# Performance work log

Hardware: AMD Instinct MI355X
Metric: run time of the kernel (lower is better)

The kernel has to match this reference:

```python
import jax, jax.numpy as jnp
import numpy as np

V, D, DFF, E, K, L = 32000, 1024, 4096, 8, 2, 2
B, S = 2, 1024


def _layer_norm(x, scale, bias, eps=1e-5):
    mu = jnp.mean(x, axis=-1, keepdims=True)
    var = jnp.var(x, axis=-1, keepdims=True)
    return (x - mu) * jax.lax.rsqrt(var + eps) * scale + bias


def setup_inputs() -> dict:
    key = jax.random.key(0)
    ks = jax.random.split(key, 16)
    s = 0.02
    return {
        "input_ids": jax.random.randint(ks[0], (B, S), 0, V, dtype=jnp.int32),
        "emb": jax.random.normal(ks[1], (V, D), jnp.float32) * s,
        "t_ln_scale": jnp.ones((L, D), jnp.float32),
        "t_ln_bias": jnp.zeros((L, D), jnp.float32),
        "t_w1": jax.random.normal(ks[2], (L, D, DFF), jnp.float32) * s,
        "t_b1": jnp.zeros((L, DFF), jnp.float32),
        "t_w2": jax.random.normal(ks[3], (L, DFF, D), jnp.float32) * s,
        "t_b2": jnp.zeros((L, D), jnp.float32),
        "Wr": jax.random.normal(ks[4], (D, E), jnp.float32) * s,
        "br": jnp.zeros((E,), jnp.float32),
        "e_w1": jax.random.normal(ks[5], (E, D, DFF), jnp.float32) * s,
        "e_b1": jnp.zeros((E, DFF), jnp.float32),
        "e_w2": jax.random.normal(ks[6], (E, DFF, D), jnp.float32) * s,
        "e_b2": jnp.zeros((E, D), jnp.float32),
        "Wl": jax.random.normal(ks[7], (D, V), jnp.float32) * s,
        "bl": jnp.zeros((V,), jnp.float32),
    }


def reference(input_ids, emb, t_ln_scale, t_ln_bias, t_w1, t_b1, t_w2, t_b2,
              Wr, br, e_w1, e_b1, e_w2, e_b2, Wl, bl):
    # token embeddings: [B,S,D]
    x = emb[input_ids]

    # temporal abstraction: L pre-LN residual MLP blocks
    for l in range(L):
        h = _layer_norm(x, t_ln_scale[l], t_ln_bias[l])
        h = jax.nn.gelu(jnp.einsum('bsd,df->bsf', h, t_w1[l]) + t_b1[l])
        x = x + jnp.einsum('bsf,fd->bsd', h, t_w2[l]) + t_b2[l]

    # router: top-k renormalized softmax over experts, scattered to [B,S,E]
    r_logits = jnp.einsum('bsd,de->bse', x, Wr) + br
    top_vals, top_idx = jax.lax.top_k(r_logits, K)
    top_w = jax.nn.softmax(top_vals, axis=-1)
    routing_weights = jnp.put_along_axis(
        jnp.zeros_like(r_logits), top_idx, top_w, axis=-1, inplace=False)

    # dense all-experts stack: [B,S,E,D]
    h = jax.nn.gelu(jnp.einsum('bsd,edf->bsef', x, e_w1) + e_b1)
    expert_out = jnp.einsum('bsef,efd->bsed', h, e_w2) + e_b2

    # sparse-weighted combine
    y = jnp.einsum('bse,bsed->bsd', routing_weights, expert_out)

    logits = jnp.einsum('bsd,dv->bsv', y, Wl) + bl
    return logits, routing_weights
```

## Files before the change

kernel.cpp:

```cpp
#include <hip/hip_runtime.h>
#include <stdint.h>

typedef __bf16 bf16;
typedef __bf16 bf16x8 __attribute__((ext_vector_type(8)));
typedef float f32x4 __attribute__((ext_vector_type(4)));

#define DEV __device__ __forceinline__

static constexpr int Dm   = 1024;
static constexpr int DFFm = 4096;
static constexpr int Tm   = 2048;
static constexpr int Vm   = 32000;

#define GLOAD_LDS16(g, l)                                                      \
  __builtin_amdgcn_global_load_lds(                                            \
      (const __attribute__((address_space(1))) unsigned int*)(g),              \
      (__attribute__((address_space(3))) unsigned int*)(l), 16, 0, 0)

DEV float gelu_tanh(float v) {
  float u = 0.7978845608028654f * (v + 0.044715f * v * v * v);
  float e = __expf(2.0f * u);
  float t = 1.0f - 2.0f / (e + 1.0f);
  return 0.5f * v * (1.0f + t);
}

enum { EPI_GELU_SPLIT = 0, EPI_RESID = 1, EPI_GELU_BF16 = 2, EPI_MOE = 3, EPI_BIAS = 4 };

struct GemmP {
  const bf16* Ah;
  const bf16* Bh;
  const float* bias;
  const float* rwp;
  const int* cnt;
  const int* idx;
  float* outF;
  bf16* outH;
  int K; int N;
  int lda; int ldb; int ldo;
  long aBS, bBS, outBS;
  int biasBS;
  int ebase;
  int kcShift; int kcK;
};

template <int EPI, bool GATHER, bool SWZ>
__launch_bounds__(256, 2)
__global__ void gemm_bt(GemmP p) {
  __shared__ bf16 lds[16384];
  bf16* ldsA = lds;
  bf16* ldsB = lds + 8192;

  const int tid  = threadIdx.x;
  const int lane = tid & 63;
  const int wid  = tid >> 6;
  const int wr   = wid >> 1;
  const int wc   = wid & 1;
  const int z    = blockIdx.z;
  const int kc   = z & ((1 << p.kcShift) - 1);
  const int ze   = z >> p.kcShift;

  int bx = blockIdx.x, by = blockIdx.y;
  if constexpr (SWZ) {
    const int gx = gridDim.x, gy = gridDim.y;
    const int nwg = gx * gy;
    const int lin = by * gx + bx;
    const int q = nwg >> 3, r = nwg & 7;
    const int xcd = lin & 7, loc = lin >> 3;
    const int nid = (xcd < r ? xcd * (q + 1) : r * (q + 1) + (xcd - r) * q) + loc;
    bx = nid / gy; by = nid % gy;
  }

  const long am0 = (long)by * 128;
  const long bn0 = (long)bx * 128;

  int cntE = 0;
  const int* il = nullptr;
  if constexpr (GATHER || EPI == EPI_MOE) {
    cntE = p.cnt[p.ebase + ze];
    if (am0 >= cntE) return;
    il = p.idx + (long)(p.ebase + ze) * 2048;
  }

  const long lda = p.lda, ldb = p.ldb;
  const long K = p.K;
  const long kco = (long)kc * p.kcK;

  const int sub = (lane & 7) ^ (lane >> 3);
  const int rIn = wid * 8 + (lane >> 3);

  const bf16 *aS[4], *bS[4];
  {
    const bf16* Bb = p.Bh + (long)ze * p.bBS + kco + bn0 * ldb;
    const bf16* Ab = p.Ah + (long)ze * p.aBS + kco + am0 * lda;
#pragma unroll
    for (int j = 0; j < 4; ++j) {
      const int row = j * 32 + rIn;
      bS[j] = Bb + (long)row * ldb + sub * 8;
      if constexpr (GATHER) {
        const int rt = (int)am0 + row;
        const long grow = il[rt < cntE ? rt : 0];
        aS[j] = p.Ah + grow * lda + kco + sub * 8;
      } else {
        aS[j] = Ab + (long)row * lda + sub * 8;
      }
    }
  }
  char* dstA[4];
#pragma unroll
  for (int j = 0; j < 4; ++j)
    dstA[j] = (char*)(void*)lds + (j * 256 + wid * 64) * 16;

  f32x4 acc[4][4] = {};

  const int r15 = lane & 15;
  const int kcs = lane >> 4;
  const int xk  = lane & 7;

  for (long k0 = 0; k0 < K; k0 += 64) {
    __syncthreads();
#pragma unroll
    for (int j = 0; j < 4; ++j) {
      GLOAD_LDS16(aS[j] + k0, dstA[j]);
      GLOAD_LDS16(bS[j] + k0, dstA[j] + 16384);
    }
    __syncthreads();
#pragma unroll
    for (int h = 0; h < 2; ++h) {
      const int q8 = ((kcs + 4 * h) ^ xk) << 3;
      bf16x8 a[4], b[4];
#pragma unroll
      for (int m = 0; m < 4; ++m)
        a[m] = *(const bf16x8*)(ldsA + (wr * 64 + m * 16 + r15) * 64 + q8);
#pragma unroll
      for (int n = 0; n < 4; ++n)
        b[n] = *(const bf16x8*)(ldsB + (wc * 64 + n * 16 + r15) * 64 + q8);
#pragma unroll
      for (int m = 0; m < 4; ++m)
#pragma unroll
        for (int n = 0; n < 4; ++n)
          acc[m][n] = __builtin_amdgcn_mfma_f32_16x16x32_bf16(a[m], b[n], acc[m][n], 0, 0, 0);
    }
  }

  const long N = p.N;

#pragma unroll
  for (int m = 0; m < 4; ++m) {
#pragma unroll
    for (int n = 0; n < 4; ++n) {
      const long col = bn0 + wc * 64 + n * 16 + (lane & 15);
      const float bv = (kc == 0) ? p.bias[(long)ze * p.biasBS + col] : 0.0f;
#pragma unroll
      for (int r = 0; r < 4; ++r) {
        const long row = am0 + wr * 64 + m * 16 + (lane >> 4) * 4 + r;
        float v = acc[m][n][r] + bv;
        if constexpr (EPI == EPI_GELU_SPLIT) {
          float g = gelu_tanh(v);
          bf16 hh = (bf16)g;
          long o = row * (long)p.ldo + col;
          p.outH[o] = hh;
          p.outH[o + N] = (bf16)(g - (float)hh);
          p.outH[o + 2 * N] = hh;
        } else if constexpr (EPI == EPI_RESID) {
          atomicAdd(p.outF + row * N + col, v);
        } else if constexpr (EPI == EPI_GELU_BF16) {
          long o = (long)ze * p.outBS + row * N + col;
          p.outH[o] = (bf16)gelu_tanh(v);
        } else if constexpr (EPI == EPI_MOE) {
          if (row < cntE) {
            const int tok = il[row];
            const float wgt = p.rwp[(long)tok * 8 + p.ebase + ze];
            atomicAdd(p.outF + (long)tok * N + col, wgt * v);
          }
        } else {
          p.outF[row * N + col] = v;
        }
      }
    }
  }
}

template <bool SWZ>
__launch_bounds__(512, 2)
__global__ void gemm256_bias(const bf16* __restrict__ A, const bf16* __restrict__ B,
                             const float* __restrict__ bias, float* __restrict__ out,
                             int Kc, int Nc) {
  __shared__ bf16 lds[65536];

  const int tid  = threadIdx.x;
  const int lane = tid & 63;
  const int wid  = tid >> 6;
  const int wr   = wid >> 2;
  const int wc   = wid & 3;

  int bx = blockIdx.x, by = blockIdx.y;
  if constexpr (SWZ) {
    const int gx = gridDim.x, gy = gridDim.y;
    const int nwg = gx * gy;
    const int lin = by * gx + bx;
    const int q = nwg >> 3, r = nwg & 7;
    const int xcd = lin & 7, loc = lin >> 3;
    const int nid = (xcd < r ? xcd * (q + 1) : r * (q + 1) + (xcd - r) * q) + loc;
    bx = nid / gy; by = nid % gy;
  }
  const long am0 = (long)by * 256;
  const long bn0 = (long)bx * 256;
  const long K = Kc;
  const int NT = Kc >> 6;

  const int sub = (lane & 7) ^ (lane >> 3);
  const int rw  = wid * 8 + (lane >> 3);
  const bf16 *aS[4], *bS[4];
#pragma unroll
  for (int j = 0; j < 4; ++j) {
    const int row = j * 64 + rw;
    aS[j] = A + (am0 + row) * K + sub * 8;
    bS[j] = B + (bn0 + row) * K + sub * 8;
  }

  f32x4 acc[8][4] = {};
  const int r15 = lane & 15;
  const int kcs = lane >> 4;
  const int xk  = lane & 7;

  auto stage = [&](int kt, int buf) {
    const long ko = (long)kt * 64;
    char* base = (char*)(void*)lds + buf * 65536;
#pragma unroll
    for (int j = 0; j < 4; ++j) {
      char* d = base + (j * 64 + wid * 8) * 128;
      GLOAD_LDS16(aS[j] + ko, d);
      GLOAD_LDS16(bS[j] + ko, d + 32768);
    }
  };

  stage(0, 0);
  stage(1, 1);

  for (int kt = 0; kt < NT; ++kt) {
    const int cur = kt & 1;
    if (kt < NT - 1) asm volatile("s_waitcnt vmcnt(8)" ::: "memory");
    else             asm volatile("s_waitcnt vmcnt(0)" ::: "memory");
    __builtin_amdgcn_s_barrier();

    const bf16* LA = lds + cur * 32768;
    const bf16* LB = LA + 16384;

    bf16x8 a0[8], b0[4];
    {
      const int q8 = (kcs ^ xk) << 3;
#pragma unroll
      for (int m = 0; m < 8; ++m)
        a0[m] = *(const bf16x8*)(LA + (wr * 128 + m * 16 + r15) * 64 + q8);
#pragma unroll
      for (int n = 0; n < 4; ++n)
        b0[n] = *(const bf16x8*)(LB + (wc * 64 + n * 16 + r15) * 64 + q8);
    }
    __builtin_amdgcn_s_setprio(1);
#pragma unroll
    for (int m = 0; m < 8; ++m)
#pragma unroll
      for (int n = 0; n < 4; ++n)
        acc[m][n] = __builtin_amdgcn_mfma_f32_16x16x32_bf16(a0[m], b0[n], acc[m][n], 0, 0, 0);
    __builtin_amdgcn_s_setprio(0);

    bf16x8 a1[8], b1[4];
    {
      const int q8 = ((kcs + 4) ^ xk) << 3;
#pragma unroll
      for (int m = 0; m < 8; ++m)
        a1[m] = *(const bf16x8*)(LA + (wr * 128 + m * 16 + r15) * 64 + q8);
#pragma unroll
      for (int n = 0; n < 4; ++n)
        b1[n] = *(const bf16x8*)(LB + (wc * 64 + n * 16 + r15) * 64 + q8);
    }
    asm volatile("s_waitcnt lgkmcnt(0)" ::: "memory");
    __builtin_amdgcn_s_barrier();
    if (kt + 2 < NT) stage(kt + 2, cur);

    __builtin_amdgcn_s_setprio(1);
#pragma unroll
    for (int m = 0; m < 8; ++m)
#pragma unroll
      for (int n = 0; n < 4; ++n)
        acc[m][n] = __builtin_amdgcn_mfma_f32_16x16x32_bf16(a1[m], b1[n], acc[m][n], 0, 0, 0);
    __builtin_amdgcn_s_setprio(0);
  }

  const long N = Nc;
#pragma unroll
  for (int m = 0; m < 8; ++m) {
#pragma unroll
    for (int n = 0; n < 4; ++n) {
      const long col = bn0 + wc * 64 + n * 16 + r15;
      const float bv = bias[col];
#pragma unroll
      for (int r = 0; r < 4; ++r) {
        const long row = am0 + wr * 128 + m * 16 + (lane >> 4) * 4 + r;
        out[row * N + col] = acc[m][n][r] + bv;
      }
    }
  }
}

template <bool AUG>
__global__ void transpose_cvt(const float* __restrict__ in, bf16* __restrict__ out,
                              int R, int C, long inBS, long outBS) {
  __shared__ float tile[32][33];
  const float* inp = in + (long)blockIdx.z * inBS;
  const long c0 = (long)blockIdx.x * 32;
  const long r0 = (long)blockIdx.y * 32;
  const int tx = threadIdx.x;
  const int ty = threadIdx.y;
#pragma unroll
  for (int i = 0; i < 4; ++i) {
    int r = ty + i * 8;
    tile[r][tx] = inp[(r0 + r) * (long)C + c0 + tx];
  }
  __syncthreads();
  const long ob = (long)blockIdx.z * outBS;
  const long stride = AUG ? 3L * R : (long)R;
#pragma unroll
  for (int i = 0; i < 4; ++i) {
    int c = ty + i * 8;
    float v = tile[tx][c];
    bf16 h = (bf16)v;
    long o = ob + (c0 + c) * stride + r0 + tx;
    out[o] = h;
    if constexpr (AUG) {
      out[o + R] = h;
      out[o + 2 * R] = (bf16)(v - (float)h);
    }
  }
}

__global__ void embed_kernel(const int* __restrict__ ids, const float* __restrict__ emb,
                             float* __restrict__ x) {
  const long t = blockIdx.x;
  const int id = ids[t];
  ((float4*)(x + t * 1024))[threadIdx.x] = ((const float4*)(emb + (long)id * 1024))[threadIdx.x];
}

__global__ void ln_aug_kernel(const float* __restrict__ x, const float* __restrict__ sc,
                              const float* __restrict__ bi, bf16* __restrict__ oa) {
  const long t = blockIdx.x;
  const int tid = threadIdx.x;
  const int lane = tid & 63, wid = tid >> 6;
  float4 a = ((const float4*)(x + t * 1024))[tid];
  float s = a.x + a.y + a.z + a.w;
  float q = a.x * a.x + a.y * a.y + a.z * a.z + a.w * a.w;
#pragma unroll
  for (int off = 32; off; off >>= 1) {
    s += __shfl_down(s, off);
    q += __shfl_down(q, off);
  }
  __shared__ float sr[4], qr[4];
  if (lane == 0) { sr[wid] = s; qr[wid] = q; }
  __syncthreads();
  s = sr[0] + sr[1] + sr[2] + sr[3];
  q = qr[0] + qr[1] + qr[2] + qr[3];
  const float mu = s * (1.0f / 1024.0f);
  const float var = q * (1.0f / 1024.0f) - mu * mu;
  const float rs = rsqrtf(var + 1e-5f);
#pragma unroll
  for (int j = 0; j < 4; ++j) {
    const int d = tid * 4 + j;
    const float g = (((const float*)&a)[j] - mu) * rs * sc[d] + bi[d];
    const bf16 h = (bf16)g;
    oa[t * 3072 + d] = h;
    oa[t * 3072 + 1024 + d] = (bf16)(g - (float)h);
    oa[t * 3072 + 2048 + d] = h;
  }
}

__global__ void router_kernel(const float* __restrict__ x, const float* __restrict__ Wr,
                              const float* __restrict__ br, float* __restrict__ rwo,
                              int* __restrict__ top2) {
  const long t = blockIdx.x;
  const int lane = threadIdx.x;
  float acc[8];
#pragma unroll
  for (int e = 0; e < 8; ++e) acc[e] = 0.0f;
  const float4* xr = (const float4*)(x + t * 1024);
#pragma unroll
  for (int j = 0; j < 4; ++j) {
    const int d4 = j * 64 + lane;
    float4 xv = xr[d4];
#pragma unroll
    for (int u = 0; u < 4; ++u) {
      const float xs = ((const float*)&xv)[u];
      const float4* wp = (const float4*)(Wr + (long)(d4 * 4 + u) * 8);
      float4 w0 = wp[0], w1 = wp[1];
      acc[0] += xs * w0.x; acc[1] += xs * w0.y; acc[2] += xs * w0.z; acc[3] += xs * w0.w;
      acc[4] += xs * w1.x; acc[5] += xs * w1.y; acc[6] += xs * w1.z; acc[7] += xs * w1.w;
    }
  }
#pragma unroll
  for (int off = 32; off; off >>= 1)
#pragma unroll
    for (int e = 0; e < 8; ++e) acc[e] += __shfl_down(acc[e], off);
  if (lane == 0) {
    float v[8];
#pragma unroll
    for (int e = 0; e < 8; ++e) v[e] = acc[e] + br[e];
    int i0 = 0; float v0 = v[0];
    for (int e = 1; e < 8; ++e) if (v[e] > v0) { v0 = v[e]; i0 = e; }
    int i1 = -1; float v1 = -3.4e38f;
    for (int e = 0; e < 8; ++e) if (e != i0 && v[e] > v1) { v1 = v[e]; i1 = e; }
    float e1 = expf(v1 - v0);
    float den = 1.0f + e1;
    float w0 = 1.0f / den, w1 = e1 / den;
    float* o = rwo + t * 8;
#pragma unroll
    for (int e = 0; e < 8; ++e) o[e] = (e == i0) ? w0 : (e == i1 ? w1 : 0.0f);
    top2[t] = i0 | (i1 << 8);
  }
}

__global__ void build_lists(const int* __restrict__ top2, int* __restrict__ cnt,
                            int* __restrict__ idx) {
  const int t = blockIdx.x * 256 + threadIdx.x;
  const int rec = top2[t];
  const int e0 = rec & 255, e1 = (rec >> 8) & 255;
  int p0 = atomicAdd(&cnt[e0], 1);
  idx[e0 * 2048 + p0] = t;
  int p1 = atomicAdd(&cnt[e1], 1);
  idx[e1 * 2048 + p1] = t;
}

__global__ void cvt_bf16_kernel(const float* __restrict__ in, bf16* __restrict__ out, long n) {
  long i = ((long)blockIdx.x * blockDim.x + threadIdx.x) * 8;
  if (i >= n) return;
  float4 a = *(const float4*)(in + i);
  float4 b = *(const float4*)(in + i + 4);
  bf16x8 o;
  o[0] = (bf16)a.x; o[1] = (bf16)a.y; o[2] = (bf16)a.z; o[3] = (bf16)a.w;
  o[4] = (bf16)b.x; o[5] = (bf16)b.y; o[6] = (bf16)b.z; o[7] = (bf16)b.w;
  *(bf16x8*)(out + i) = o;
}

extern "C" void kernel_launch(void* const* d_in, const int* in_sizes, int n_in,
                              void* d_out, int out_size, void* d_ws, size_t ws_size,
                              hipStream_t stream) {
  (void)in_sizes; (void)n_in; (void)out_size; (void)ws_size;
  const int*   ids  = (const int*)d_in[0];
  const float* emb  = (const float*)d_in[1];
  const float* tlns = (const float*)d_in[2];
  const float* tlnb = (const float*)d_in[3];
  const float* tw1  = (const float*)d_in[4];
  const float* tb1  = (const float*)d_in[5];
  const float* tw2  = (const float*)d_in[6];
  const float* tb2  = (const float*)d_in[7];
  const float* Wr   = (const float*)d_in[8];
  const float* br   = (const float*)d_in[9];
  const float* ew1  = (const float*)d_in[10];
  const float* eb1  = (const float*)d_in[11];
  const float* ew2  = (const float*)d_in[12];
  const float* eb2  = (const float*)d_in[13];
  const float* Wl   = (const float*)d_in[14];
  const float* bl   = (const float*)d_in[15];

  float* logits = (float*)d_out;
  float* rwout  = (float*)d_out + (long)Tm * Vm;

  size_t off = 0;
  auto take = [&](size_t bytes) {
    void* pp = (char*)d_ws + off;
    off += (bytes + 255) & ~(size_t)255;
    return pp;
  };
  float* X    = (float*)take((size_t)Tm * Dm * 4);
  bf16*  XB   = (bf16*) take((size_t)Tm * Dm * 2);
  float* Y    = (float*)take((size_t)Tm * Dm * 4);
  bf16*  YB   = (bf16*) take((size_t)Tm * Dm * 2);
  int*   top2 = (int*)  take((size_t)Tm * 4);
  int*   cnt  = (int*)  take(8 * 4);
  int*   idxl = (int*)  take((size_t)8 * Tm * 4);
  char*  S    = (char*) take(134217728);

  bf16* A1  = (bf16*)S;
  bf16* W1A = (bf16*)(S + 12582912);
  bf16* W2A = (bf16*)(S + 12582912 + 25165824);
  bf16* HTA = (bf16*)(S + 12582912 + 2 * 25165824);
  bf16* EW1T = (bf16*)S;
  bf16* HE   = (bf16*)(S + 33554432);
  bf16* EW2T = (bf16*)(S + 100663296);
  bf16* WLT  = (bf16*)S;

  embed_kernel<<<dim3(Tm), dim3(256), 0, stream>>>(ids, emb, X);

  for (int l = 0; l < 2; ++l) {
    transpose_cvt<true><<<dim3(DFFm / 32, Dm / 32, 1), dim3(32, 8), 0, stream>>>(
        tw1 + (long)l * Dm * DFFm, W1A, Dm, DFFm, 0, 0);
    transpose_cvt<true><<<dim3(Dm / 32, DFFm / 32, 1), dim3(32, 8), 0, stream>>>(
        tw2 + (long)l * DFFm * Dm, W2A, DFFm, Dm, 0, 0);
    ln_aug_kernel<<<dim3(Tm), dim3(256), 0, stream>>>(X, tlns + l * Dm, tlnb + l * Dm, A1);

    GemmP p1{};
    p1.Ah = A1; p1.Bh = W1A;
    p1.bias = tb1 + (long)l * DFFm;
    p1.outH = HTA;
    p1.K = 3072; p1.N = DFFm; p1.lda = 3072; p1.ldb = 3072; p1.ldo = 3 * DFFm;
    gemm_bt<EPI_GELU_SPLIT, false, true>
        <<<dim3(DFFm / 128, Tm / 128, 1), dim3(256), 0, stream>>>(p1);

    GemmP p2{};
    p2.Ah = HTA; p2.Bh = W2A;
    p2.bias = tb2 + (long)l * Dm;
    p2.outF = X;
    p2.K = 1536; p2.N = Dm; p2.lda = 12288; p2.ldb = 12288;
    p2.kcShift = 3; p2.kcK = 1536;
    gemm_bt<EPI_RESID, false, true>
        <<<dim3(Dm / 128, Tm / 128, 8), dim3(256), 0, stream>>>(p2);
  }

  router_kernel<<<dim3(Tm), dim3(64), 0, stream>>>(X, Wr, br, rwout, top2);
  hipMemsetAsync(cnt, 0, 8 * 4, stream);
  build_lists<<<dim3(Tm / 256), dim3(256), 0, stream>>>(top2, cnt, idxl);
  cvt_bf16_kernel<<<dim3(Tm * Dm / (256 * 8)), dim3(256), 0, stream>>>(X, XB, (long)Tm * Dm);
  hipMemsetAsync(Y, 0, (size_t)Tm * Dm * 4, stream);

  for (int q = 0; q < 2; ++q) {
    transpose_cvt<false><<<dim3(DFFm / 32, Dm / 32, 4), dim3(32, 8), 0, stream>>>(
        ew1 + (long)q * 4 * Dm * DFFm, EW1T, Dm, DFFm, (long)Dm * DFFm, (long)DFFm * Dm);
    transpose_cvt<false><<<dim3(Dm / 32, DFFm / 32, 4), dim3(32, 8), 0, stream>>>(
        ew2 + (long)q * 4 * DFFm * Dm, EW2T, DFFm, Dm, (long)DFFm * Dm, (long)Dm * DFFm);

    GemmP pe1{};
    pe1.Ah = XB; pe1.Bh = EW1T;
    pe1.bias = eb1 + (long)q * 4 * DFFm; pe1.biasBS = DFFm;
    pe1.outH = HE; pe1.outBS = (long)Tm * DFFm;
    pe1.aBS = 0; pe1.bBS = (long)DFFm * Dm;
    pe1.cnt = cnt; pe1.idx = idxl; pe1.ebase = q * 4;
    pe1.K = Dm; pe1.N = DFFm; pe1.lda = Dm; pe1.ldb = Dm;
    gemm_bt<EPI_GELU_BF16, true, true>
        <<<dim3(DFFm / 128, Tm / 128, 4), dim3(256), 0, stream>>>(pe1);

    GemmP pe2{};
    pe2.Ah = HE; pe2.aBS = (long)Tm * DFFm;
    pe2.Bh = EW2T; pe2.bBS = (long)Dm * DFFm;
    pe2.bias = eb2 + (long)q * 4 * Dm; pe2.biasBS = Dm;
    pe2.rwp = rwout; pe2.cnt = cnt; pe2.idx = idxl; pe2.ebase = q * 4;
    pe2.outF = Y;
    pe2.K = 1024; pe2.N = Dm; pe2.lda = DFFm; pe2.ldb = DFFm;
    pe2.kcShift = 2; pe2.kcK = 1024;
    gemm_bt<EPI_MOE, false, true>
        <<<dim3(Dm / 128, Tm / 128, 16), dim3(256), 0, stream>>>(pe2);
  }

  cvt_bf16_kernel<<<dim3(Tm * Dm / (256 * 8)), dim3(256), 0, stream>>>(Y, YB, (long)Tm * Dm);
  transpose_cvt<false><<<dim3(Vm / 32, Dm / 32, 1), dim3(32, 8), 0, stream>>>(
      Wl, WLT, Dm, Vm, 0, 0);
  gemm256_bias<true><<<dim3(Vm / 256, Tm / 256, 1), dim3(512), 0, stream>>>(
      YB, WLT, bl, logits, Dm, Vm);
}
```

Measured before the change: 980.5 us.

## Move temporal MLP GEMMs to 256-tile kernel with two-term split-bf16 operands

Replaces the 3-way augmented split-bf16 scheme (hi, lo, hi) with a 2-way layout (hi, lo). Virtual K-index remapping lets the GEMM pair A-hi/lo against B-hi twice, which cuts the stored operand width. The temporal MLP GEMMs move to a generalized 256x256-tile kernel with split-K atomics. The first GEMM now writes fp32 to a zeroed scratch buffer, followed by a separate GELU+split pass. This adds a memset and an extra round trip through memory for the activation, and the staging loop is restructured into half-K stages with finer-grained waits.

```diff
diff --git a/kernel.cpp b/kernel.cpp
--- a/kernel.cpp
+++ b/kernel.cpp
@@ -24,7 +24,165 @@
   return 0.5f * v * (1.0f + t);
 }
 
-enum { EPI_GELU_SPLIT = 0, EPI_RESID = 1, EPI_GELU_BF16 = 2, EPI_MOE = 3, EPI_BIAS = 4 };
+struct G256P {
+  const bf16* A; const bf16* B;
+  const float* bias;
+  float* outF;
+  int K;
+  int N;
+  int lda; int ldb;
+  int kcK;
+  int aT, aS2, bT, bS2;
+};
+
+template <int EPI , bool SWZ>
+__launch_bounds__(512, 2)
+__global__ void gemm256(G256P p) {
+  __shared__ bf16 lds[65536];
+  const int tid  = threadIdx.x;
+  const int lane = tid & 63;
+  const int wid  = tid >> 6;
+  const int wr   = wid >> 2;
+  const int wc   = wid & 3;
+  const int kc   = blockIdx.z;
+
+  int bx = blockIdx.x, by = blockIdx.y;
+  if constexpr (SWZ) {
+    const int gx = gridDim.x, gy = gridDim.y;
+    const int nwg = gx * gy;
+    const int lin = by * gx + bx;
+    const int q = nwg >> 3, r = nwg & 7;
+    const int xcd = lin & 7, loc = lin >> 3;
+    const int nid = (xcd < r ? xcd * (q + 1) : r * (q + 1) + (xcd - r) * q) + loc;
+    bx = nid / gy; by = nid % gy;
+  }
+  const long am0 = (long)by * 256;
+  const long bn0 = (long)bx * 256;
+  const long lda = p.lda, ldb = p.ldb;
+  const int kco = kc * p.kcK;
+  const int NT = p.K >> 6;
+
+  const int v = (lane & 7) ^ (lane >> 3);
+  const long arow = 2 * (wid * 8 + (lane >> 3)) + (v >> 2);
+  const bf16* aR0 = p.A + (am0 + arow) * lda + (v & 3) * 8;
+  const bf16* aR1 = aR0 + 128 * lda;
+  const bf16* bR0 = p.B + (bn0 + arow) * ldb + (v & 3) * 8;
+  const bf16* bR1 = bR0 + 128 * ldb;
+  char* ldsc = (char*)(void*)lds;
+
+  auto stageA = [&](int kt, int kh) {
+    const int ku = kco + kt * 64 + kh * 32;
+    const long ka = (ku >= p.aT) ? ku - p.aS2 : ku;
+    char* d = ldsc + (kt & 1) * 65536 + kh * 32768 + wid * 1024;
+    GLOAD_LDS16(aR0 + ka, d);
+    GLOAD_LDS16(aR1 + ka, d + 8192);
+  };
+  auto stageB = [&](int kt, int kh) {
+    const int ku = kco + kt * 64 + kh * 32;
+    const long kb = (ku >= p.bT) ? ku - p.bS2 : ku;
+    char* d = ldsc + (kt & 1) * 65536 + kh * 32768 + 16384 + wid * 1024;
+    GLOAD_LDS16(bR0 + kb, d);
+    GLOAD_LDS16(bR1 + kb, d + 8192);
+  };
+
+  f32x4 acc[8][4] = {};
+  const int r15 = lane & 15;
+  const int kcs = lane >> 4;
+  const int boff = (r15 >> 1) * 128 +
+                   (((((r15 & 1) << 2) | kcs) ^ ((r15 >> 1) & 7)) << 4);
+
+  stageA(0, 0); stageB(0, 0); stageA(0, 1); stageB(0, 1);
+  stageA(1, 0); stageB(1, 0); stageA(1, 1); stageB(1, 1);
+
+  for (int t = 0; t < NT; ++t) {
+    const char* buf = ldsc + (t & 1) * 65536;
+    const bool st = (t >= 1) && (t + 1 < NT);
+
+    if (t == 0) asm volatile("s_waitcnt vmcnt(12)" ::: "memory");
+    else        asm volatile("s_waitcnt vmcnt(4)" ::: "memory");
+    __builtin_amdgcn_s_barrier();
+    {
+      const char* Ab = buf + boff + wr * 8192;
+      const char* Bb = buf + 16384 + boff + wc * 4096;
+      bf16x8 a[4], b[4];
+#pragma unroll
+      for (int n = 0; n < 4; ++n) b[n] = *(const bf16x8*)(Bb + n * 1024);
+#pragma unroll
+      for (int m = 0; m < 4; ++m) a[m] = *(const bf16x8*)(Ab + m * 1024);
+      if (st) stageA(t + 1, 0);
+      __builtin_amdgcn_s_setprio(1);
+#pragma unroll
+      for (int m = 0; m < 4; ++m)
+#pragma unroll
+        for (int n = 0; n < 4; ++n)
+          acc[m][n] = __builtin_amdgcn_mfma_f32_16x16x32_bf16(a[m], b[n], acc[m][n], 0, 0, 0);
+      __builtin_amdgcn_s_setprio(0);
+#pragma unroll
+      for (int m = 0; m < 4; ++m) a[m] = *(const bf16x8*)(Ab + 4096 + m * 1024);
+      if (st) stageB(t + 1, 0);
+      __builtin_amdgcn_s_setprio(1);
+#pragma unroll
+      for (int m = 0; m < 4; ++m)
+#pragma unroll
+        for (int n = 0; n < 4; ++n)
+          acc[4 + m][n] = __builtin_amdgcn_mfma_f32_16x16x32_bf16(a[m], b[n], acc[4 + m][n], 0, 0, 0);
+      __builtin_amdgcn_s_setprio(0);
+    }
+
+    if (t == 0)           asm volatile("s_waitcnt vmcnt(8)" ::: "memory");
+    else if (t == NT - 1) asm volatile("s_waitcnt vmcnt(0)" ::: "memory");
+    else                  asm volatile("s_waitcnt vmcnt(4)" ::: "memory");
+    __builtin_amdgcn_s_barrier();
+    {
+      const char* Ab = buf + 32768 + boff + wr * 8192;
+      const char* Bb = buf + 32768 + 16384 + boff + wc * 4096;
+      bf16x8 a[4], b[4];
+#pragma unroll
+      for (int n = 0; n < 4; ++n) b[n] = *(const bf16x8*)(Bb + n * 1024);
+#pragma unroll
+      for (int m = 0; m < 4; ++m) a[m] = *(const bf16x8*)(Ab + m * 1024);
+      if (st) stageA(t + 1, 1);
+      __builtin_amdgcn_s_setprio(1);
+#pragma unroll
+      for (int m = 0; m < 4; ++m)
+#pragma unroll
+        for (int n = 0; n < 4; ++n)
+          acc[m][n] = __builtin_amdgcn_mfma_f32_16x16x32_bf16(a[m], b[n], acc[m][n], 0, 0, 0);
+      __builtin_amdgcn_s_setprio(0);
+#pragma unroll
+      for (int m = 0; m < 4; ++m) a[m] = *(const bf16x8*)(Ab + 4096 + m * 1024);
+      if (st) stageB(t + 1, 1);
+      __builtin_amdgcn_s_setprio(1);
+#pragma unroll
+      for (int m = 0; m < 4; ++m)
+#pragma unroll
+        for (int n = 0; n < 4; ++n)
+          acc[4 + m][n] = __builtin_amdgcn_mfma_f32_16x16x32_bf16(a[m], b[n], acc[4 + m][n], 0, 0, 0);
+      __builtin_amdgcn_s_setprio(0);
+    }
+  }
+
+  const long N = p.N;
+#pragma unroll
+  for (int m = 0; m < 8; ++m) {
+#pragma unroll
+    for (int n = 0; n < 4; ++n) {
+      const long col = bn0 + wc * 64 + n * 16 + r15;
+      const float bv = (EPI == 0 || kc == 0) ? p.bias[col] : 0.0f;
+#pragma unroll
+      for (int r = 0; r < 4; ++r) {
+        const long row = am0 + wr * 128 + m * 16 + (lane >> 4) * 4 + r;
+        if constexpr (EPI == 0) {
+          p.outF[row * N + col] = acc[m][n][r] + bv;
+        } else {
+          atomicAdd(p.outF + row * N + col, acc[m][n][r] + bv);
+        }
+      }
+    }
+  }
+}
+
+enum { EPI_GELU_BF16 = 2, EPI_MOE = 3 };
 
 struct GemmP {
   const bf16* Ah;
@@ -36,7 +194,7 @@
   float* outF;
   bf16* outH;
   int K; int N;
-  int lda; int ldb; int ldo;
+  int lda; int ldb;
   long aBS, bBS, outBS;
   int biasBS;
   int ebase;
@@ -143,7 +301,6 @@
   }
 
   const long N = p.N;
-
 #pragma unroll
   for (int m = 0; m < 4; ++m) {
 #pragma unroll
@@ -154,156 +311,22 @@
       for (int r = 0; r < 4; ++r) {
         const long row = am0 + wr * 64 + m * 16 + (lane >> 4) * 4 + r;
         float v = acc[m][n][r] + bv;
-        if constexpr (EPI == EPI_GELU_SPLIT) {
-          float g = gelu_tanh(v);
-          bf16 hh = (bf16)g;
-          long o = row * (long)p.ldo + col;
-          p.outH[o] = hh;
-          p.outH[o + N] = (bf16)(g - (float)hh);
-          p.outH[o + 2 * N] = hh;
-        } else if constexpr (EPI == EPI_RESID) {
-          atomicAdd(p.outF + row * N + col, v);
-        } else if constexpr (EPI == EPI_GELU_BF16) {
+        if constexpr (EPI == EPI_GELU_BF16) {
           long o = (long)ze * p.outBS + row * N + col;
           p.outH[o] = (bf16)gelu_tanh(v);
-        } else if constexpr (EPI == EPI_MOE) {
+        } else {
           if (row < cntE) {
             const int tok = il[row];
             const float wgt = p.rwp[(long)tok * 8 + p.ebase + ze];
             atomicAdd(p.outF + (long)tok * N + col, wgt * v);
           }
-        } else {
-          p.outF[row * N + col] = v;
         }
       }
     }
   }
 }
 
-template <bool SWZ>
-__launch_bounds__(512, 2)
-__global__ void gemm256_bias(const bf16* __restrict__ A, const bf16* __restrict__ B,
-                             const float* __restrict__ bias, float* __restrict__ out,
-                             int Kc, int Nc) {
-  __shared__ bf16 lds[65536];
-
-  const int tid  = threadIdx.x;
-  const int lane = tid & 63;
-  const int wid  = tid >> 6;
-  const int wr   = wid >> 2;
-  const int wc   = wid & 3;
-
-  int bx = blockIdx.x, by = blockIdx.y;
-  if constexpr (SWZ) {
-    const int gx = gridDim.x, gy = gridDim.y;
-    const int nwg = gx * gy;
-    const int lin = by * gx + bx;
-    const int q = nwg >> 3, r = nwg & 7;
-    const int xcd = lin & 7, loc = lin >> 3;
-    const int nid = (xcd < r ? xcd * (q + 1) : r * (q + 1) + (xcd - r) * q) + loc;
-    bx = nid / gy; by = nid % gy;
-  }
-  const long am0 = (long)by * 256;
-  const long bn0 = (long)bx * 256;
-  const long K = Kc;
-  const int NT = Kc >> 6;
-
-  const int sub = (lane & 7) ^ (lane >> 3);
-  const int rw  = wid * 8 + (lane >> 3);
-  const bf16 *aS[4], *bS[4];
-#pragma unroll
-  for (int j = 0; j < 4; ++j) {
-    const int row = j * 64 + rw;
-    aS[j] = A + (am0 + row) * K + sub * 8;
-    bS[j] = B + (bn0 + row) * K + sub * 8;
-  }
-
-  f32x4 acc[8][4] = {};
-  const int r15 = lane & 15;
-  const int kcs = lane >> 4;
-  const int xk  = lane & 7;
-
-  auto stage = [&](int kt, int buf) {
-    const long ko = (long)kt * 64;
-    char* base = (char*)(void*)lds + buf * 65536;
-#pragma unroll
-    for (int j = 0; j < 4; ++j) {
-      char* d = base + (j * 64 + wid * 8) * 128;
-      GLOAD_LDS16(aS[j] + ko, d);
-      GLOAD_LDS16(bS[j] + ko, d + 32768);
-    }
-  };
-
-  stage(0, 0);
-  stage(1, 1);
-
-  for (int kt = 0; kt < NT; ++kt) {
-    const int cur = kt & 1;
-    if (kt < NT - 1) asm volatile("s_waitcnt vmcnt(8)" ::: "memory");
-    else             asm volatile("s_waitcnt vmcnt(0)" ::: "memory");
-    __builtin_amdgcn_s_barrier();
-
-    const bf16* LA = lds + cur * 32768;
-    const bf16* LB = LA + 16384;
-
-    bf16x8 a0[8], b0[4];
-    {
-      const int q8 = (kcs ^ xk) << 3;
-#pragma unroll
-      for (int m = 0; m < 8; ++m)
-        a0[m] = *(const bf16x8*)(LA + (wr * 128 + m * 16 + r15) * 64 + q8);
-#pragma unroll
-      for (int n = 0; n < 4; ++n)
-        b0[n] = *(const bf16x8*)(LB + (wc * 64 + n * 16 + r15) * 64 + q8);
-    }
-    __builtin_amdgcn_s_setprio(1);
-#pragma unroll
-    for (int m = 0; m < 8; ++m)
-#pragma unroll
-      for (int n = 0; n < 4; ++n)
-        acc[m][n] = __builtin_amdgcn_mfma_f32_16x16x32_bf16(a0[m], b0[n], acc[m][n], 0, 0, 0);
-    __builtin_amdgcn_s_setprio(0);
-
-    bf16x8 a1[8], b1[4];
-    {
-      const int q8 = ((kcs + 4) ^ xk) << 3;
-#pragma unroll
-      for (int m = 0; m < 8; ++m)
-        a1[m] = *(const bf16x8*)(LA + (wr * 128 + m * 16 + r15) * 64 + q8);
-#pragma unroll
-      for (int n = 0; n < 4; ++n)
-        b1[n] = *(const bf16x8*)(LB + (wc * 64 + n * 16 + r15) * 64 + q8);
-    }
-    asm volatile("s_waitcnt lgkmcnt(0)" ::: "memory");
-    __builtin_amdgcn_s_barrier();
-    if (kt + 2 < NT) stage(kt + 2, cur);
-
-    __builtin_amdgcn_s_setprio(1);
-#pragma unroll
-    for (int m = 0; m < 8; ++m)
-#pragma unroll
-      for (int n = 0; n < 4; ++n)
-        acc[m][n] = __builtin_amdgcn_mfma_f32_16x16x32_bf16(a1[m], b1[n], acc[m][n], 0, 0, 0);
-    __builtin_amdgcn_s_setprio(0);
-  }
-
-  const long N = Nc;
-#pragma unroll
-  for (int m = 0; m < 8; ++m) {
-#pragma unroll
-    for (int n = 0; n < 4; ++n) {
-      const long col = bn0 + wc * 64 + n * 16 + r15;
-      const float bv = bias[col];
-#pragma unroll
-      for (int r = 0; r < 4; ++r) {
-        const long row = am0 + wr * 128 + m * 16 + (lane >> 4) * 4 + r;
-        out[row * N + col] = acc[m][n][r] + bv;
-      }
-    }
-  }
-}
-
-template <bool AUG>
+template <bool AUG2>
 __global__ void transpose_cvt(const float* __restrict__ in, bf16* __restrict__ out,
                               int R, int C, long inBS, long outBS) {
   __shared__ float tile[32][33];
@@ -319,7 +342,7 @@
   }
   __syncthreads();
   const long ob = (long)blockIdx.z * outBS;
-  const long stride = AUG ? 3L * R : (long)R;
+  const long stride = AUG2 ? 2L * R : (long)R;
 #pragma unroll
   for (int i = 0; i < 4; ++i) {
     int c = ty + i * 8;
@@ -327,10 +350,7 @@
     bf16 h = (bf16)v;
     long o = ob + (c0 + c) * stride + r0 + tx;
     out[o] = h;
-    if constexpr (AUG) {
-      out[o + R] = h;
-      out[o + 2 * R] = (bf16)(v - (float)h);
-    }
+    if constexpr (AUG2) out[o + R] = (bf16)(v - (float)h);
   }
 }
 
@@ -341,8 +361,8 @@
   ((float4*)(x + t * 1024))[threadIdx.x] = ((const float4*)(emb + (long)id * 1024))[threadIdx.x];
 }
 
-__global__ void ln_aug_kernel(const float* __restrict__ x, const float* __restrict__ sc,
-                              const float* __restrict__ bi, bf16* __restrict__ oa) {
+__global__ void ln_aug2_kernel(const float* __restrict__ x, const float* __restrict__ sc,
+                               const float* __restrict__ bi, bf16* __restrict__ oa) {
   const long t = blockIdx.x;
   const int tid = threadIdx.x;
   const int lane = tid & 63, wid = tid >> 6;
@@ -367,10 +387,26 @@
     const int d = tid * 4 + j;
     const float g = (((const float*)&a)[j] - mu) * rs * sc[d] + bi[d];
     const bf16 h = (bf16)g;
-    oa[t * 3072 + d] = h;
-    oa[t * 3072 + 1024 + d] = (bf16)(g - (float)h);
-    oa[t * 3072 + 2048 + d] = h;
-  }
+    oa[t * 2048 + d] = h;
+    oa[t * 2048 + 1024 + d] = (bf16)(g - (float)h);
+  }
+}
+
+__global__ void gelu_aug2_kernel(const float* __restrict__ Z, bf16* __restrict__ H) {
+  const long i8 = ((long)blockIdx.x * 256 + threadIdx.x) * 8;
+  const long r = i8 >> 12, c = i8 & 4095;
+  float4 a = *(const float4*)(Z + i8);
+  float4 b = *(const float4*)(Z + i8 + 4);
+  bf16x8 h, l;
+#pragma unroll
+  for (int j = 0; j < 8; ++j) {
+    float g = gelu_tanh(j < 4 ? ((const float*)&a)[j] : ((const float*)&b)[j - 4]);
+    bf16 hh = (bf16)g;
+    h[j] = hh;
+    l[j] = (bf16)(g - (float)hh);
+  }
+  *(bf16x8*)(H + r * 8192 + c) = h;
+  *(bf16x8*)(H + r * 8192 + 4096 + c) = l;
 }
 
 __global__ void router_kernel(const float* __restrict__ x, const float* __restrict__ Wr,
@@ -478,10 +514,11 @@
   int*   idxl = (int*)  take((size_t)8 * Tm * 4);
   char*  S    = (char*) take(134217728);
 
-  bf16* A1  = (bf16*)S;
-  bf16* W1A = (bf16*)(S + 12582912);
-  bf16* W2A = (bf16*)(S + 12582912 + 25165824);
-  bf16* HTA = (bf16*)(S + 12582912 + 2 * 25165824);
+  bf16*  A1  = (bf16*)S;
+  bf16*  W1A = (bf16*)(S + 8388608);
+  bf16*  W2A = (bf16*)(S + 25165824);
+  float* Z   = (float*)(S + 41943040);
+  bf16*  HTA = (bf16*)(S + 75497472);
   bf16* EW1T = (bf16*)S;
   bf16* HE   = (bf16*)(S + 33554432);
   bf16* EW2T = (bf16*)(S + 100663296);
@@ -494,24 +531,22 @@
         tw1 + (long)l * Dm * DFFm, W1A, Dm, DFFm, 0, 0);
     transpose_cvt<true><<<dim3(Dm / 32, DFFm / 32, 1), dim3(32, 8), 0, stream>>>(
         tw2 + (long)l * DFFm * Dm, W2A, DFFm, Dm, 0, 0);
-    ln_aug_kernel<<<dim3(Tm), dim3(256), 0, stream>>>(X, tlns + l * Dm, tlnb + l * Dm, A1);
-
-    GemmP p1{};
-    p1.Ah = A1; p1.Bh = W1A;
-    p1.bias = tb1 + (long)l * DFFm;
-    p1.outH = HTA;
-    p1.K = 3072; p1.N = DFFm; p1.lda = 3072; p1.ldb = 3072; p1.ldo = 3 * DFFm;
-    gemm_bt<EPI_GELU_SPLIT, false, true>
-        <<<dim3(DFFm / 128, Tm / 128, 1), dim3(256), 0, stream>>>(p1);
-
-    GemmP p2{};
-    p2.Ah = HTA; p2.Bh = W2A;
-    p2.bias = tb2 + (long)l * Dm;
-    p2.outF = X;
-    p2.K = 1536; p2.N = Dm; p2.lda = 12288; p2.ldb = 12288;
-    p2.kcShift = 3; p2.kcK = 1536;
-    gemm_bt<EPI_RESID, false, true>
-        <<<dim3(Dm / 128, Tm / 128, 8), dim3(256), 0, stream>>>(p2);
+    ln_aug2_kernel<<<dim3(Tm), dim3(256), 0, stream>>>(X, tlns + l * Dm, tlnb + l * Dm, A1);
+    hipMemsetAsync(Z, 0, (size_t)Tm * DFFm * 4, stream);
+
+    G256P p1{};
+    p1.A = A1; p1.B = W1A; p1.bias = tb1 + (long)l * DFFm; p1.outF = Z;
+    p1.K = 1536; p1.N = DFFm; p1.lda = 2048; p1.ldb = 2048; p1.kcK = 1536;
+    p1.aT = 2048; p1.aS2 = 2048; p1.bT = 1024; p1.bS2 = 1024;
+    gemm256<1, true><<<dim3(DFFm / 256, Tm / 256, 2), dim3(512), 0, stream>>>(p1);
+
+    gelu_aug2_kernel<<<dim3(Tm * DFFm / (256 * 8)), dim3(256), 0, stream>>>(Z, HTA);
+
+    G256P p2{};
+    p2.A = HTA; p2.B = W2A; p2.bias = tb2 + (long)l * Dm; p2.outF = X;
+    p2.K = 1536; p2.N = Dm; p2.lda = 8192; p2.ldb = 8192; p2.kcK = 1536;
+    p2.aT = 8192; p2.aS2 = 8192; p2.bT = 4096; p2.bS2 = 4096;
+    gemm256<1, true><<<dim3(Dm / 256, Tm / 256, 8), dim3(512), 0, stream>>>(p2);
   }
 
   router_kernel<<<dim3(Tm), dim3(64), 0, stream>>>(X, Wr, br, rwout, top2);
@@ -551,6 +586,9 @@
   cvt_bf16_kernel<<<dim3(Tm * Dm / (256 * 8)), dim3(256), 0, stream>>>(Y, YB, (long)Tm * Dm);
   transpose_cvt<false><<<dim3(Vm / 32, Dm / 32, 1), dim3(32, 8), 0, stream>>>(
       Wl, WLT, Dm, Vm, 0, 0);
-  gemm256_bias<true><<<dim3(Vm / 256, Tm / 256, 1), dim3(512), 0, stream>>>(
-      YB, WLT, bl, logits, Dm, Vm);
-}
+  G256P pl{};
+  pl.A = YB; pl.B = WLT; pl.bias = bl; pl.outF = logits;
+  pl.K = Dm; pl.N = Vm; pl.lda = Dm; pl.ldb = Dm; pl.kcK = 0;
+  pl.aT = 1 << 30; pl.aS2 = 0; pl.bT = 1 << 30; pl.bS2 = 0;
+  gemm256<0, true><<<dim3(Vm / 256, Tm / 256, 1), dim3(512), 0, stream>>>(pl);
+}
```

Result: slower. 1.118 ms (+14.0%).

## Rewrite LM-head GEMM as an 8-phase interleaved load/MFMA pipeline

Applied to the files above, without the earlier changes.

Replaces the 256x256 LM-head GEMM kernel with a variant that splits each k-tile into four phases. Each phase loads two A fragments from LDS, issues part of the next tile's global-to-LDS loads, and runs a block of MFMAs, with barriers between phases. The aim is to spread global loads and LDS reads across the MFMA work instead of bunching them, which should hide latency and lower register pressure. The cost is many more barriers per tile and a more fragile vmcnt accounting. It also removes the unused EPI_BIAS path.

```diff
diff --git a/kernel.cpp b/kernel.cpp
--- a/kernel.cpp
+++ b/kernel.cpp
@@ -24,7 +24,184 @@
   return 0.5f * v * (1.0f + t);
 }
 
-enum { EPI_GELU_SPLIT = 0, EPI_RESID = 1, EPI_GELU_BF16 = 2, EPI_MOE = 3, EPI_BIAS = 4 };
+template <bool SWZ>
+__launch_bounds__(512, 2)
+__global__ void gemm256_8p(const bf16* __restrict__ A, const bf16* __restrict__ B,
+                           const float* __restrict__ bias, float* __restrict__ out,
+                           int Kc, int Nc) {
+  __shared__ bf16 lds[65536];
+  const int tid  = threadIdx.x;
+  const int lane = tid & 63;
+  const int wid  = tid >> 6;
+  const int wr   = wid >> 2;
+  const int wc   = wid & 3;
+
+  int bx = blockIdx.x, by = blockIdx.y;
+  if constexpr (SWZ) {
+    const int gx = gridDim.x, gy = gridDim.y;
+    const int nwg = gx * gy;
+    const int lin = by * gx + bx;
+    const int q = nwg >> 3, r = nwg & 7;
+    const int xcd = lin & 7, loc = lin >> 3;
+    const int nid = (xcd < r ? xcd * (q + 1) : r * (q + 1) + (xcd - r) * q) + loc;
+    bx = nid / gy; by = nid % gy;
+  }
+  const long am0 = (long)by * 256;
+  const long bn0 = (long)bx * 256;
+  const long K = Kc;
+  const int NT = Kc >> 6;
+
+  const int sub = (lane & 7) ^ (lane >> 3);
+  const int rw  = wid * 8 + (lane >> 3);
+  const bf16 *aS[4], *bS[4];
+#pragma unroll
+  for (int j = 0; j < 4; ++j) {
+    aS[j] = A + (am0 + j * 64 + rw) * K + sub * 8;
+    bS[j] = B + (bn0 + j * 64 + rw) * K + sub * 8;
+  }
+  char* ldsc = (char*)(void*)lds;
+
+#define STG_A(kt, j)                                                           \
+  GLOAD_LDS16(aS[j] + (long)(kt) * 64,                                         \
+              ldsc + ((kt) & 1) * 65536 + ((j) * 64 + wid * 8) * 128)
+#define STG_B(kt, j)                                                           \
+  GLOAD_LDS16(bS[j] + (long)(kt) * 64,                                         \
+              ldsc + ((kt) & 1) * 65536 + 32768 + ((j) * 64 + wid * 8) * 128)
+
+  STG_B(0, 0); STG_B(0, 1); STG_B(0, 2); STG_B(0, 3);
+  STG_A(0, 0); STG_A(0, 2); STG_A(0, 1); STG_A(0, 3);
+  if (NT > 1) {
+    STG_B(1, 0); STG_B(1, 1); STG_B(1, 2); STG_B(1, 3);
+    STG_A(1, 0); STG_A(1, 2);
+    asm volatile("s_waitcnt vmcnt(6)" ::: "memory");
+  } else {
+    asm volatile("s_waitcnt vmcnt(0)" ::: "memory");
+  }
+  __builtin_amdgcn_s_barrier();
+
+  f32x4 acc[8][4] = {};
+  const int r15 = lane & 15;
+  const int kcs = lane >> 4;
+  const int x7  = lane & 7;
+  const int q80 = (kcs ^ x7) << 3;
+  const int q81 = ((kcs + 4) ^ x7) << 3;
+
+  for (int t = 0; t < NT; ++t) {
+    const bf16* LAb = lds + (t & 1) * 32768 + wr * 128 * 64;
+    const bf16* LBb = lds + (t & 1) * 32768 + 16384 + wc * 64 * 64;
+    bf16x8 b0[4], b1[4];
+
+    {
+      bf16x8 a0, a1, a2, a3;
+#pragma unroll
+      for (int n = 0; n < 4; ++n) {
+        b0[n] = *(const bf16x8*)(LBb + (n * 16 + r15) * 64 + q80);
+        b1[n] = *(const bf16x8*)(LBb + (n * 16 + r15) * 64 + q81);
+      }
+      a0 = *(const bf16x8*)(LAb + (0 * 16 + r15) * 64 + q80);
+      a1 = *(const bf16x8*)(LAb + (0 * 16 + r15) * 64 + q81);
+      a2 = *(const bf16x8*)(LAb + (1 * 16 + r15) * 64 + q80);
+      a3 = *(const bf16x8*)(LAb + (1 * 16 + r15) * 64 + q81);
+      if (t + 1 < NT) { STG_A(t + 1, 1); STG_A(t + 1, 3); }
+      __builtin_amdgcn_s_barrier();
+      asm volatile("s_waitcnt lgkmcnt(0)" ::: "memory");
+      __builtin_amdgcn_s_setprio(1);
+#pragma unroll
+      for (int n = 0; n < 4; ++n) {
+        acc[0][n] = __builtin_amdgcn_mfma_f32_16x16x32_bf16(a0, b0[n], acc[0][n], 0, 0, 0);
+        acc[0][n] = __builtin_amdgcn_mfma_f32_16x16x32_bf16(a1, b1[n], acc[0][n], 0, 0, 0);
+        acc[1][n] = __builtin_amdgcn_mfma_f32_16x16x32_bf16(a2, b0[n], acc[1][n], 0, 0, 0);
+        acc[1][n] = __builtin_amdgcn_mfma_f32_16x16x32_bf16(a3, b1[n], acc[1][n], 0, 0, 0);
+      }
+      __builtin_amdgcn_s_setprio(0);
+      __builtin_amdgcn_s_barrier();
+    }
+    {
+      bf16x8 a0, a1, a2, a3;
+      a0 = *(const bf16x8*)(LAb + (2 * 16 + r15) * 64 + q80);
+      a1 = *(const bf16x8*)(LAb + (2 * 16 + r15) * 64 + q81);
+      a2 = *(const bf16x8*)(LAb + (3 * 16 + r15) * 64 + q80);
+      a3 = *(const bf16x8*)(LAb + (3 * 16 + r15) * 64 + q81);
+      if (t + 2 < NT) { STG_B(t + 2, 0); STG_B(t + 2, 1); }
+      __builtin_amdgcn_s_barrier();
+      asm volatile("s_waitcnt lgkmcnt(0)" ::: "memory");
+      __builtin_amdgcn_s_setprio(1);
+#pragma unroll
+      for (int n = 0; n < 4; ++n) {
+        acc[2][n] = __builtin_amdgcn_mfma_f32_16x16x32_bf16(a0, b0[n], acc[2][n], 0, 0, 0);
+        acc[2][n] = __builtin_amdgcn_mfma_f32_16x16x32_bf16(a1, b1[n], acc[2][n], 0, 0, 0);
+        acc[3][n] = __builtin_amdgcn_mfma_f32_16x16x32_bf16(a2, b0[n], acc[3][n], 0, 0, 0);
+        acc[3][n] = __builtin_amdgcn_mfma_f32_16x16x32_bf16(a3, b1[n], acc[3][n], 0, 0, 0);
+      }
+      __builtin_amdgcn_s_setprio(0);
+      __builtin_amdgcn_s_barrier();
+    }
+    {
+      bf16x8 a0, a1, a2, a3;
+      a0 = *(const bf16x8*)(LAb + (4 * 16 + r15) * 64 + q80);
+      a1 = *(const bf16x8*)(LAb + (4 * 16 + r15) * 64 + q81);
+      a2 = *(const bf16x8*)(LAb + (5 * 16 + r15) * 64 + q80);
+      a3 = *(const bf16x8*)(LAb + (5 * 16 + r15) * 64 + q81);
+      if (t + 2 < NT) { STG_B(t + 2, 2); STG_B(t + 2, 3); }
+      __builtin_amdgcn_s_barrier();
+      asm volatile("s_waitcnt lgkmcnt(0)" ::: "memory");
+      __builtin_amdgcn_s_setprio(1);
+#pragma unroll
+      for (int n = 0; n < 4; ++n) {
+        acc[4][n] = __builtin_amdgcn_mfma_f32_16x16x32_bf16(a0, b0[n], acc[4][n], 0, 0, 0);
+        acc[4][n] = __builtin_amdgcn_mfma_f32_16x16x32_bf16(a1, b1[n], acc[4][n], 0, 0, 0);
+        acc[5][n] = __builtin_amdgcn_mfma_f32_16x16x32_bf16(a2, b0[n], acc[5][n], 0, 0, 0);
+        acc[5][n] = __builtin_amdgcn_mfma_f32_16x16x32_bf16(a3, b1[n], acc[5][n], 0, 0, 0);
+      }
+      __builtin_amdgcn_s_setprio(0);
+      __builtin_amdgcn_s_barrier();
+    }
+    {
+      bf16x8 a0, a1, a2, a3;
+      a0 = *(const bf16x8*)(LAb + (6 * 16 + r15) * 64 + q80);
+      a1 = *(const bf16x8*)(LAb + (6 * 16 + r15) * 64 + q81);
+      a2 = *(const bf16x8*)(LAb + (7 * 16 + r15) * 64 + q80);
+      a3 = *(const bf16x8*)(LAb + (7 * 16 + r15) * 64 + q81);
+      if (t + 2 < NT) {
+        STG_A(t + 2, 0); STG_A(t + 2, 2);
+        asm volatile("s_waitcnt vmcnt(6)" ::: "memory");
+      } else if (t + 1 < NT) {
+        asm volatile("s_waitcnt vmcnt(0)" ::: "memory");
+      }
+      __builtin_amdgcn_s_barrier();
+      asm volatile("s_waitcnt lgkmcnt(0)" ::: "memory");
+      __builtin_amdgcn_s_setprio(1);
+#pragma unroll
+      for (int n = 0; n < 4; ++n) {
+        acc[6][n] = __builtin_amdgcn_mfma_f32_16x16x32_bf16(a0, b0[n], acc[6][n], 0, 0, 0);
+        acc[6][n] = __builtin_amdgcn_mfma_f32_16x16x32_bf16(a1, b1[n], acc[6][n], 0, 0, 0);
+        acc[7][n] = __builtin_amdgcn_mfma_f32_16x16x32_bf16(a2, b0[n], acc[7][n], 0, 0, 0);
+        acc[7][n] = __builtin_amdgcn_mfma_f32_16x16x32_bf16(a3, b1[n], acc[7][n], 0, 0, 0);
+      }
+      __builtin_amdgcn_s_setprio(0);
+      __builtin_amdgcn_s_barrier();
+    }
+  }
+#undef STG_A
+#undef STG_B
+
+  const long N = Nc;
+#pragma unroll
+  for (int m = 0; m < 8; ++m) {
+#pragma unroll
+    for (int n = 0; n < 4; ++n) {
+      const long col = bn0 + wc * 64 + n * 16 + r15;
+      const float bv = bias[col];
+#pragma unroll
+      for (int r = 0; r < 4; ++r) {
+        const long row = am0 + wr * 128 + m * 16 + (lane >> 4) * 4 + r;
+        out[row * N + col] = acc[m][n][r] + bv;
+      }
+    }
+  }
+}
+
+enum { EPI_GELU_SPLIT = 0, EPI_RESID = 1, EPI_GELU_BF16 = 2, EPI_MOE = 3 };
 
 struct GemmP {
   const bf16* Ah;
@@ -143,7 +320,6 @@
   }
 
   const long N = p.N;
-
 #pragma unroll
   for (int m = 0; m < 4; ++m) {
 #pragma unroll
@@ -172,132 +348,7 @@
             const float wgt = p.rwp[(long)tok * 8 + p.ebase + ze];
             atomicAdd(p.outF + (long)tok * N + col, wgt * v);
           }
-        } else {
-          p.outF[row * N + col] = v;
         }
-      }
-    }
-  }
-}
-
-template <bool SWZ>
-__launch_bounds__(512, 2)
-__global__ void gemm256_bias(const bf16* __restrict__ A, const bf16* __restrict__ B,
-                             const float* __restrict__ bias, float* __restrict__ out,
-                             int Kc, int Nc) {
-  __shared__ bf16 lds[65536];
-
-  const int tid  = threadIdx.x;
-  const int lane = tid & 63;
-  const int wid  = tid >> 6;
-  const int wr   = wid >> 2;
-  const int wc   = wid & 3;
-
-  int bx = blockIdx.x, by = blockIdx.y;
-  if constexpr (SWZ) {
-    const int gx = gridDim.x, gy = gridDim.y;
-    const int nwg = gx * gy;
-    const int lin = by * gx + bx;
-    const int q = nwg >> 3, r = nwg & 7;
-    const int xcd = lin & 7, loc = lin >> 3;
-    const int nid = (xcd < r ? xcd * (q + 1) : r * (q + 1) + (xcd - r) * q) + loc;
-    bx = nid / gy; by = nid % gy;
-  }
-  const long am0 = (long)by * 256;
-  const long bn0 = (long)bx * 256;
-  const long K = Kc;
-  const int NT = Kc >> 6;
-
-  const int sub = (lane & 7) ^ (lane >> 3);
-  const int rw  = wid * 8 + (lane >> 3);
-  const bf16 *aS[4], *bS[4];
-#pragma unroll
-  for (int j = 0; j < 4; ++j) {
-    const int row = j * 64 + rw;
-    aS[j] = A + (am0 + row) * K + sub * 8;
-    bS[j] = B + (bn0 + row) * K + sub * 8;
-  }
-
-  f32x4 acc[8][4] = {};
-  const int r15 = lane & 15;
-  const int kcs = lane >> 4;
-  const int xk  = lane & 7;
-
-  auto stage = [&](int kt, int buf) {
-    const long ko = (long)kt * 64;
-    char* base = (char*)(void*)lds + buf * 65536;
-#pragma unroll
-    for (int j = 0; j < 4; ++j) {
-      char* d = base + (j * 64 + wid * 8) * 128;
-      GLOAD_LDS16(aS[j] + ko, d);
-      GLOAD_LDS16(bS[j] + ko, d + 32768);
-    }
-  };
-
-  stage(0, 0);
-  stage(1, 1);
-
-  for (int kt = 0; kt < NT; ++kt) {
-    const int cur = kt & 1;
-    if (kt < NT - 1) asm volatile("s_waitcnt vmcnt(8)" ::: "memory");
-    else             asm volatile("s_waitcnt vmcnt(0)" ::: "memory");
-    __builtin_amdgcn_s_barrier();
-
-    const bf16* LA = lds + cur * 32768;
-    const bf16* LB = LA + 16384;
-
-    bf16x8 a0[8], b0[4];
-    {
-      const int q8 = (kcs ^ xk) << 3;
-#pragma unroll
-      for (int m = 0; m < 8; ++m)
-        a0[m] = *(const bf16x8*)(LA + (wr * 128 + m * 16 + r15) * 64 + q8);
-#pragma unroll
-      for (int n = 0; n < 4; ++n)
-        b0[n] = *(const bf16x8*)(LB + (wc * 64 + n * 16 + r15) * 64 + q8);
-    }
-    __builtin_amdgcn_s_setprio(1);
-#pragma unroll
-    for (int m = 0; m < 8; ++m)
-#pragma unroll
-      for (int n = 0; n < 4; ++n)
-        acc[m][n] = __builtin_amdgcn_mfma_f32_16x16x32_bf16(a0[m], b0[n], acc[m][n], 0, 0, 0);
-    __builtin_amdgcn_s_setprio(0);
-
-    bf16x8 a1[8], b1[4];
-    {
-      const int q8 = ((kcs + 4) ^ xk) << 3;
-#pragma unroll
-      for (int m = 0; m < 8; ++m)
-        a1[m] = *(const bf16x8*)(LA + (wr * 128 + m * 16 + r15) * 64 + q8);
-#pragma unroll
-      for (int n = 0; n < 4; ++n)
-        b1[n] = *(const bf16x8*)(LB + (wc * 64 + n * 16 + r15) * 64 + q8);
-    }
-    asm volatile("s_waitcnt lgkmcnt(0)" ::: "memory");
-    __builtin_amdgcn_s_barrier();
-    if (kt + 2 < NT) stage(kt + 2, cur);
-
-    __builtin_amdgcn_s_setprio(1);
-#pragma unroll
-    for (int m = 0; m < 8; ++m)
-#pragma unroll
-      for (int n = 0; n < 4; ++n)
-        acc[m][n] = __builtin_amdgcn_mfma_f32_16x16x32_bf16(a1[m], b1[n], acc[m][n], 0, 0, 0);
-    __builtin_amdgcn_s_setprio(0);
-  }
-
-  const long N = Nc;
-#pragma unroll
-  for (int m = 0; m < 8; ++m) {
-#pragma unroll
-    for (int n = 0; n < 4; ++n) {
-      const long col = bn0 + wc * 64 + n * 16 + r15;
-      const float bv = bias[col];
-#pragma unroll
-      for (int r = 0; r < 4; ++r) {
-        const long row = am0 + wr * 128 + m * 16 + (lane >> 4) * 4 + r;
-        out[row * N + col] = acc[m][n][r] + bv;
       }
     }
   }
@@ -551,6 +602,6 @@
   cvt_bf16_kernel<<<dim3(Tm * Dm / (256 * 8)), dim3(256), 0, stream>>>(Y, YB, (long)Tm * Dm);
   transpose_cvt<false><<<dim3(Vm / 32, Dm / 32, 1), dim3(32, 8), 0, stream>>>(
       Wl, WLT, Dm, Vm, 0, 0);
-  gemm256_bias<true><<<dim3(Vm / 256, Tm / 256, 1), dim3(512), 0, stream>>>(
+  gemm256_8p<true><<<dim3(Vm / 256, Tm / 256, 1), dim3(512), 0, stream>>>(
       YB, WLT, bl, logits, Dm, Vm);
 }
```

Result: no change. 979.7 us (-0.1%).
